# Kernel optimization log

Measured on AMD Instinct MI355X. Metric: run time of the kernel, lower is better.

## Reference

```python
import jax, jax.numpy as jnp
import numpy as np

B, L, D_MODEL = 8, 2048, 768
D_INNER, D_STATE, DT_RANK, K = 1536, 16, 48, 4


def setup_inputs() -> dict:
    key = jax.random.key(0)
    ks = jax.random.split(key, 9)
    s = 0.02
    return {
        "hidden_states": jax.random.normal(ks[0], (B, L, D_MODEL), jnp.float32),
        "W_in": jax.random.normal(ks[1], (D_MODEL, 2 * D_INNER), jnp.float32) * s,
        "conv_w": jax.random.normal(ks[2], (D_INNER, 1, K), jnp.float32) * s,
        "conv_b": jax.random.normal(ks[3], (D_INNER,), jnp.float32) * s,
        "W_x": jax.random.normal(ks[4], (DT_RANK + 2 * D_STATE, D_INNER), jnp.float32) * s,
        "W_dt": jax.random.normal(ks[5], (D_INNER, DT_RANK), jnp.float32) * s,
        "b_dt": jax.random.normal(ks[6], (D_INNER,), jnp.float32) * s,
        "A_log": jax.random.normal(ks[7], (D_INNER, D_STATE), jnp.float32),
        "D_param": jax.random.normal(ks[8], (D_INNER,), jnp.float32),
    }


def _mamba(hidden_states, W_in, conv_w, conv_b, W_x, W_dt, b_dt, A_log, D_param):
    # in_proj then chunk into ssm branch (x) and gating residual (res)
    xz = hidden_states @ W_in                      # (B, L, 2*d_inner)
    x, res = jnp.split(xz, 2, axis=-1)             # each (B, L, d_inner)

    # causal depthwise conv over time, then SiLU
    xc = x.transpose(0, 2, 1)                      # (B, C, L)
    xc = jax.lax.conv_general_dilated(
        xc, conv_w, window_strides=(1,), padding=[(K - 1, 0)],
        feature_group_count=D_INNER, dimension_numbers=("NCH", "OIH", "NCH"))
    x = jax.nn.silu(xc + conv_b[None, :, None]).transpose(0, 2, 1)  # (B, L, d_inner)

    # input-dependent SSM parameters
    x_dbl = x @ W_x.T                              # (B, L, dt_rank + 2*d_state)
    dt = jax.nn.softplus(x_dbl[..., :DT_RANK] @ W_dt.T + b_dt)      # (B, L, d_inner)
    Bm = x_dbl[..., DT_RANK:DT_RANK + D_STATE]     # (B, L, d_state)
    Cm = x_dbl[..., DT_RANK + D_STATE:]            # (B, L, d_state)
    A = -jnp.exp(A_log)                            # (d_inner, d_state)

    def step(h, inp):
        x_t, dt_t, B_t, C_t = inp                  # (B,d_inner),(B,d_inner),(B,d_state),(B,d_state)
        dA = jnp.exp(dt_t[..., None] * A)          # (B, d_inner, d_state)
        dBx = (dt_t * x_t)[..., None] * B_t[:, None, :]
        h = dA * h + dBx
        y = jnp.einsum("bds,bs->bd", h, C_t)
        return h, y

    xs = (x.transpose(1, 0, 2), dt.transpose(1, 0, 2),
          Bm.transpose(1, 0, 2), Cm.transpose(1, 0, 2))
    h0 = jnp.zeros((x.shape[0], D_INNER, D_STATE), x.dtype)
    _, ys = jax.lax.scan(step, h0, xs)             # ys: (L, B, d_inner)
    y = ys.transpose(1, 0, 2) + x * D_param        # skip term
    return y * jax.nn.silu(res)                    # gated output (B, L, d_inner)


def reference(hidden_states, W_in, conv_w, conv_b, W_x, W_dt, b_dt, A_log, D_param):
    return _mamba(hidden_states, W_in, conv_w, conv_b, W_x, W_dt, b_dt, A_log, D_param)
```

## Files before the change

### kernel.cpp

```cpp
#include <hip/hip_runtime.h>
#include <hip/hip_bf16.h>
#include <stdint.h>

#define B_SZ 8
#define L_SZ 2048
#define DM 768
#define DI 1536
#define DS 16
#define DR 48
#define M_SZ (B_SZ * L_SZ)
#define N1 (2 * DI)

#define NC 32
#define TC (L_SZ / NC)
#define CH (B_SZ * DI)
#define KS 6
#define NT (DM / 64)
#define L2E 1.44269504088896f

typedef short short8 __attribute__((ext_vector_type(8)));
typedef float f32x4 __attribute__((ext_vector_type(4)));
typedef float f32x2 __attribute__((ext_vector_type(2)));

__device__ __forceinline__ ushort f2b(float f) {
  __hip_bfloat16 h = __float2bfloat16(f);
  return *reinterpret_cast<ushort*>(&h);
}
__device__ __forceinline__ float b2f(ushort u) {
  __hip_bfloat16 h;
  *reinterpret_cast<ushort*>(&h) = u;
  return __bfloat162float(h);
}
__device__ __forceinline__ ushort f2h(float f) {
  _Float16 h = (_Float16)f;
  return *reinterpret_cast<ushort*>(&h);
}
__device__ __forceinline__ float h2f(ushort u) {
  _Float16 h;
  *reinterpret_cast<ushort*>(&h) = u;
  return (float)h;
}

__device__ __forceinline__ void gl16(const ushort* g, ushort* l) {
  __builtin_amdgcn_global_load_lds(
      (const __attribute__((address_space(1))) void*)g,
      (__attribute__((address_space(3))) void*)l, 16, 0, 0);
}


__global__ __launch_bounds__(256) void prep_all(const float4* __restrict__ hs4,
                                                const float* __restrict__ w_in,
                                                const float* __restrict__ wx_f,
                                                const float* __restrict__ wdt_f,
                                                ushort4* __restrict__ A1,
                                                ushort* __restrict__ wt,
                                                ushort* __restrict__ wx_b,
                                                ushort* __restrict__ wdt_p) {
  const int n4 = M_SZ * DM / 4;
  const int nT = 3072 * 96;
  const int nwx = 80 * DI;
  const int nwdt = DI * 64;
  int idx = blockIdx.x * 256 + threadIdx.x;
  if (idx < n4) {
    float4 v = hs4[idx];
    ushort4 o;
    o.x = f2b(v.x); o.y = f2b(v.y); o.z = f2b(v.z); o.w = f2b(v.w);
    A1[idx] = o;
  } else if (idx < n4 + nT) {
    int j = idx - n4;
    int n = j % 3072;
    int kb = (j / 3072) * 8;
    short8 o;
#pragma unroll
    for (int q = 0; q < 8; ++q) o[q] = (short)f2b(w_in[(size_t)(kb + q) * 3072 + n]);
    *(short8*)(wt + (size_t)n * DM + kb) = o;
  } else if (idx < n4 + nT + nwx) {
    int j = idx - n4 - nT;
    wx_b[j] = f2b(wx_f[j]);
  } else if (idx < n4 + nT + nwx + nwdt) {
    int j = idx - n4 - nT - nwx;
    int col = j >> 6, k = j & 63;
    wdt_p[j] = (k < DR) ? f2b(wdt_f[col * DR + k]) : (ushort)0;
  }
}


__global__ __launch_bounds__(512, 1) void gemm_xz(const ushort* __restrict__ A,
                                                  const ushort* __restrict__ Bt,
                                                  ushort* __restrict__ xout,
                                                  ushort* __restrict__ gateout) {
  __shared__ ushort lds[65536];

  const int t = threadIdx.x;
  const int lane = t & 63;
  const int wid = t >> 6;
  const int wm = wid >> 2, wn = wid & 3;
  const int r = lane & 15, hi = lane >> 4;

  const int g = blockIdx.x;
  const int swz = (g & 7) * (768 / 8) + (g >> 3);
  const int bx = swz & 63;
  const int by = swz >> 6;
  const int bm = bx * 256;
  const int bn = by * 256;

  const bool isA = wid < 4;
  const int w4 = wid & 3;
  const ushort* gsrc[8];
  int ldso[8];
#pragma unroll
  for (int i = 0; i < 8; ++i) {
    int c = w4 * 8 + i;
    int mg = c >> 1, kkc = c & 1;
    gsrc[i] = (isA ? A + (size_t)(bm + mg * 16 + r) * DM
                   : Bt + (size_t)(bn + mg * 16 + r) * DM) + kkc * 32 + hi * 8;
    ldso[i] = (isA ? 0 : 16384) + c * 512;
  }

  f32x4 acc[8][4];
#pragma unroll
  for (int m = 0; m < 8; ++m)
#pragma unroll
    for (int n = 0; n < 4; ++n) acc[m][n] = f32x4{0.f, 0.f, 0.f, 0.f};

#pragma unroll
  for (int i = 0; i < 8; ++i) gl16(gsrc[i], &lds[ldso[i]]);
  asm volatile("s_waitcnt vmcnt(0)" ::: "memory");
  __builtin_amdgcn_s_barrier();

  for (int kt = 0; kt < NT; ++kt) {
    const int cur = kt & 1;
    const ushort* bufA = &lds[cur * 32768];
    const ushort* bufB = bufA + 16384;
    ushort* nxt = &lds[(cur ^ 1) * 32768];
    const int koff = (kt + 1) * 64;
    const bool more = (kt + 1 < NT);

    short8 afr[4][2], bfr[2][2];
#pragma unroll
    for (int q = 0; q < 4; ++q) {
      const int mq = q >> 1, nq = q & 1;
      if (nq == 0) {
#pragma unroll
        for (int m = 0; m < 4; ++m)
#pragma unroll
          for (int kk = 0; kk < 2; ++kk)
            afr[m][kk] = *(const short8*)&bufA[((wm * 8 + mq * 4 + m) * 2 + kk) * 512 + lane * 8];
      }
#pragma unroll
      for (int n = 0; n < 2; ++n)
#pragma unroll
        for (int kk = 0; kk < 2; ++kk)
          bfr[n][kk] = *(const short8*)&bufB[((wn * 4 + nq * 2 + n) * 2 + kk) * 512 + lane * 8];

      if (more) {
        gl16(gsrc[2 * q] + koff, nxt + ldso[2 * q]);
        gl16(gsrc[2 * q + 1] + koff, nxt + ldso[2 * q + 1]);
      }

      asm volatile("s_barrier" ::: "memory");

      __builtin_amdgcn_s_setprio(1);
#pragma unroll
      for (int m = 0; m < 4; ++m)
#pragma unroll
        for (int n = 0; n < 2; ++n) {
          f32x4 a = acc[mq * 4 + m][nq * 2 + n];
          a = __builtin_amdgcn_mfma_f32_16x16x32_bf16(afr[m][0], bfr[n][0], a, 0, 0, 0);
          a = __builtin_amdgcn_mfma_f32_16x16x32_bf16(afr[m][1], bfr[n][1], a, 0, 0, 0);
          acc[mq * 4 + m][nq * 2 + n] = a;
        }
      __builtin_amdgcn_s_setprio(0);

      if (q == 3) asm volatile("s_waitcnt vmcnt(0)" ::: "memory");
      asm volatile("s_barrier" ::: "memory");
    }
  }

  const bool isx = (bn < DI);
  ushort* outp = isx ? xout : gateout;
  const int cbase = bn - (isx ? 0 : DI) + wn * 64;
#pragma unroll
  for (int mf = 0; mf < 8; ++mf)
#pragma unroll
    for (int nf = 0; nf < 4; ++nf) {
      int col = cbase + nf * 16 + r;
#pragma unroll
      for (int j = 0; j < 4; ++j) {
        int row = bm + wm * 128 + mf * 16 + hi * 4 + j;
        float v = acc[mf][nf][j];
        if (!isx) v = v / (1.f + __expf(-v));
        outp[(size_t)row * DI + col] = f2b(v);
      }
    }
}


__global__ __launch_bounds__(256) void conv_silu(const ushort* __restrict__ xp,
                                                 const float* __restrict__ cw,
                                                 const float* __restrict__ cb,
                                                 ushort* __restrict__ xc) {
  int tid = blockIdx.x * 256 + threadIdx.x;
  const int nd = DI / 8;
  int db = tid % nd;
  int row = tid / nd;
  int d0 = db * 8;
  int l = row & (L_SZ - 1);
  const ushort* base = xp + (size_t)row * DI + d0;
  short8 z8 = {0, 0, 0, 0, 0, 0, 0, 0};
  short8 x0 = *(const short8*)base;
  short8 xm1 = (l >= 1) ? *(const short8*)(base - DI) : z8;
  short8 xm2 = (l >= 2) ? *(const short8*)(base - 2 * DI) : z8;
  short8 xm3 = (l >= 3) ? *(const short8*)(base - 3 * DI) : z8;
  short8 o;
#pragma unroll
  for (int j = 0; j < 8; ++j) {
    float4 w = *(const float4*)(cw + (size_t)(d0 + j) * 4);
    float a = cb[d0 + j] + w.x * b2f((ushort)xm3[j]) + w.y * b2f((ushort)xm2[j]) +
              w.z * b2f((ushort)xm1[j]) + w.w * b2f((ushort)x0[j]);
    float s = a / (1.f + __expf(-a));
    o[j] = (short)f2b(s);
  }
  *(short8*)(xc + (size_t)row * DI + d0) = o;
}


__global__ __launch_bounds__(256) void xdbl_gemm(const ushort* __restrict__ xc,
                                                 const ushort* __restrict__ wx,
                                                 float* __restrict__ xdp) {
  int wave = blockIdx.x * 4 + (threadIdx.x >> 6);
  int ks = blockIdx.y;
  int lane = threadIdx.x & 63;
  int r = lane & 15, hi = lane >> 4;
  int row0 = wave * 16;
  f32x4 acc[5];
#pragma unroll
  for (int n = 0; n < 5; ++n) acc[n] = f32x4{0.f, 0.f, 0.f, 0.f};
  const int kbeg = ks * (DI / KS), kend = kbeg + DI / KS;
  for (int k0 = kbeg; k0 < kend; k0 += 32) {
    short8 a = *(const short8*)(xc + (size_t)(row0 + r) * DI + k0 + hi * 8);
#pragma unroll
    for (int n = 0; n < 5; ++n) {
      short8 b = *(const short8*)(wx + (size_t)(n * 16 + r) * DI + k0 + hi * 8);
      acc[n] = __builtin_amdgcn_mfma_f32_16x16x32_bf16(a, b, acc[n], 0, 0, 0);
    }
  }
  float* op = xdp + (size_t)ks * M_SZ * 80;
#pragma unroll
  for (int n = 0; n < 5; ++n)
#pragma unroll
    for (int j = 0; j < 4; ++j)
      op[(size_t)(row0 + hi * 4 + j) * 80 + n * 16 + r] = acc[n][j];
}

__global__ __launch_bounds__(256) void reduce_xd(const float4* __restrict__ xdp,
                                                 float4* __restrict__ xd) {
  int i = blockIdx.x * 256 + threadIdx.x;
  if (i >= M_SZ * 20) return;
  float4 s = xdp[i];
#pragma unroll
  for (int k = 1; k < KS; ++k) {
    float4 v = xdp[(size_t)k * M_SZ * 20 + i];
    s.x += v.x; s.y += v.y; s.z += v.z; s.w += v.w;
  }
  xd[i] = s;
}


__device__ __forceinline__ short8 pack8f(const float* p) {
  short8 v;
#pragma unroll
  for (int i = 0; i < 8; ++i) v[i] = (short)f2b(p[i]);
  return v;
}

__global__ __launch_bounds__(256) void dt_gemm(const float* __restrict__ xd,
                                               const ushort* __restrict__ wdtp,
                                               const float* __restrict__ bdt,
                                               ushort* __restrict__ dt) {
  int wave = blockIdx.x * 4 + (threadIdx.x >> 6);
  int lane = threadIdx.x & 63;
  int r = lane & 15, hi = lane >> 4;
  int row0 = wave * 16;
  int c0 = blockIdx.y * 64;

  float atmp[8];
  const float* ap = xd + (size_t)(row0 + r) * 80 + hi * 8;
  float4 q0 = *(const float4*)ap, q1 = *(const float4*)(ap + 4);
  atmp[0] = q0.x; atmp[1] = q0.y; atmp[2] = q0.z; atmp[3] = q0.w;
  atmp[4] = q1.x; atmp[5] = q1.y; atmp[6] = q1.z; atmp[7] = q1.w;
  short8 a0 = pack8f(atmp);
  short8 a1 = {0, 0, 0, 0, 0, 0, 0, 0};
  if (hi < 2) {
    const float* ap1 = xd + (size_t)(row0 + r) * 80 + 32 + hi * 8;
    float4 p0 = *(const float4*)ap1, p1 = *(const float4*)(ap1 + 4);
    atmp[0] = p0.x; atmp[1] = p0.y; atmp[2] = p0.z; atmp[3] = p0.w;
    atmp[4] = p1.x; atmp[5] = p1.y; atmp[6] = p1.z; atmp[7] = p1.w;
    a1 = pack8f(atmp);
  }

  f32x4 acc[4];
#pragma unroll
  for (int n = 0; n < 4; ++n) acc[n] = f32x4{0.f, 0.f, 0.f, 0.f};
#pragma unroll
  for (int n = 0; n < 4; ++n) {
    const ushort* wp = wdtp + (size_t)(c0 + n * 16 + r) * 64;
    short8 b0 = *(const short8*)(wp + hi * 8);
    short8 b1 = *(const short8*)(wp + 32 + hi * 8);
    acc[n] = __builtin_amdgcn_mfma_f32_16x16x32_bf16(a0, b0, acc[n], 0, 0, 0);
    acc[n] = __builtin_amdgcn_mfma_f32_16x16x32_bf16(a1, b1, acc[n], 0, 0, 0);
  }
#pragma unroll
  for (int n = 0; n < 4; ++n)
#pragma unroll
    for (int j = 0; j < 4; ++j) {
      int col = c0 + n * 16 + r;
      float z = acc[n][j] + bdt[col];
      float sp = (z > 20.f) ? z : __logf(1.f + __expf(z));
      dt[(size_t)(row0 + hi * 4 + j) * DI + col] = f2h(sp);
    }
}


__global__ __launch_bounds__(256) void scan_pass1(const ushort* __restrict__ dt,
                                                  const ushort* __restrict__ xc,
                                                  const float* __restrict__ xd,
                                                  const float* __restrict__ A_log,
                                                  float* __restrict__ hend,
                                                  float* __restrict__ sumdt) {
  const int d = blockIdx.x * 256 + threadIdx.x;
  const int c = blockIdx.y, b = blockIdx.z;
  const int t0 = c * TC;

  __shared__ float Bs[TC * 16];
  for (int i = threadIdx.x; i < TC * 16; i += 256) {
    int tt = i >> 4, s = i & 15;
    Bs[i] = xd[((size_t)(b * L_SZ + t0 + tt)) * 80 + DR + s];
  }

  f32x2 a2[8];
  const float4* al4 = (const float4*)(A_log + (size_t)d * DS);
#pragma unroll
  for (int q = 0; q < 4; ++q) {
    float4 v = al4[q];
    a2[2 * q] = f32x2{-__expf(v.x) * L2E, -__expf(v.y) * L2E};
    a2[2 * q + 1] = f32x2{-__expf(v.z) * L2E, -__expf(v.w) * L2E};
  }

  __syncthreads();

  f32x2 h2[8];
#pragma unroll
  for (int s = 0; s < 8; ++s) h2[s] = f32x2{0.f, 0.f};
  float sd = 0.f;

  const ushort* dtp = dt + ((size_t)b * L_SZ + t0) * DI + d;
  const ushort* xp = xc + ((size_t)b * L_SZ + t0) * DI + d;

  ushort dtu_n = dtp[0];
  ushort xu_n = xp[0];
  for (int tt = 0; tt < TC; ++tt) {
    ushort dtu = dtu_n;
    ushort xu = xu_n;
    dtu_n = dtp[(size_t)(tt + 1) * DI];
    xu_n = xp[(size_t)(tt + 1) * DI];
    float dtv = h2f(dtu);
    float xv = b2f(xu);
    sd += dtv;
    float dx = dtv * xv;
    f32x2 dt2 = f32x2{dtv, dtv};
    f32x2 dx2 = f32x2{dx, dx};
    const f32x2* bp2 = (const f32x2*)&Bs[tt * 16];
#pragma unroll
    for (int sp = 0; sp < 8; ++sp) {
      f32x2 arg = dt2 * a2[sp];
      float e0, e1;
      asm("v_exp_f32 %0, %1" : "=v"(e0) : "v"(arg[0]));
      asm("v_exp_f32 %0, %1" : "=v"(e1) : "v"(arg[1]));
      f32x2 dA = f32x2{e0, e1};
      h2[sp] = dA * h2[sp] + dx2 * bp2[sp];
    }
  }

  const size_t ch = (size_t)b * DI + d;
  sumdt[ch * NC + c] = sd;
  float4* hp = (float4*)&hend[((size_t)c * CH + ch) * 16];
#pragma unroll
  for (int q = 0; q < 4; ++q)
    hp[q] = make_float4(h2[2 * q][0], h2[2 * q][1], h2[2 * q + 1][0], h2[2 * q + 1][1]);
}

__global__ __launch_bounds__(256) void scan_pass2(const float* __restrict__ A_log,
                                                  const float* __restrict__ sumdt,
                                                  const float* __restrict__ hend,
                                                  float* __restrict__ hstart) {
  int idx = blockIdx.x * 256 + threadIdx.x;
  int ch = idx >> 4, s = idx & 15;
  int d = ch % DI;
  float A = -__expf(A_log[d * DS + s]);
  float h = 0.f;
  for (int c = 0; c < NC; ++c) {
    hstart[((size_t)c * CH + ch) * 16 + s] = h;
    float sd = sumdt[(size_t)ch * NC + c];
    h = __expf(A * sd) * h + hend[((size_t)c * CH + ch) * 16 + s];
  }
}

__global__ __launch_bounds__(256) void scan_pass3(const ushort* __restrict__ dt,
                                                  const ushort* __restrict__ xc,
                                                  const float* __restrict__ xd,
                                                  const ushort* __restrict__ gateb,
                                                  const float* __restrict__ A_log,
                                                  const float* __restrict__ Dp,
                                                  const float* __restrict__ hstart,
                                                  float* __restrict__ out) {
  const int d = blockIdx.x * 256 + threadIdx.x;
  const int c = blockIdx.y, b = blockIdx.z;
  const int t0 = c * TC;

  __shared__ float Bs[TC * 16];
  __shared__ float Cs[TC * 16];
  for (int i = threadIdx.x; i < TC * 16; i += 256) {
    int tt = i >> 4, s = i & 15;
    size_t row = ((size_t)(b * L_SZ + t0 + tt)) * 80;
    Bs[i] = xd[row + DR + s];
    Cs[i] = xd[row + DR + DS + s];
  }

  f32x2 a2[8];
  const float4* al4 = (const float4*)(A_log + (size_t)d * DS);
#pragma unroll
  for (int q = 0; q < 4; ++q) {
    float4 v = al4[q];
    a2[2 * q] = f32x2{-__expf(v.x) * L2E, -__expf(v.y) * L2E};
    a2[2 * q + 1] = f32x2{-__expf(v.z) * L2E, -__expf(v.w) * L2E};
  }
  const float Dpv = Dp[d];

  const size_t ch = (size_t)b * DI + d;
  f32x2 h2[8];
  const float4* hp = (const float4*)&hstart[((size_t)c * CH + ch) * 16];
#pragma unroll
  for (int q = 0; q < 4; ++q) {
    float4 v = hp[q];
    h2[2 * q] = f32x2{v.x, v.y};
    h2[2 * q + 1] = f32x2{v.z, v.w};
  }

  __syncthreads();

  const ushort* dtp = dt + ((size_t)b * L_SZ + t0) * DI + d;
  const ushort* xp = xc + ((size_t)b * L_SZ + t0) * DI + d;
  const ushort* gp = gateb + ((size_t)b * L_SZ + t0) * DI + d;
  float* op = out + ((size_t)b * L_SZ + t0) * DI + d;

  ushort dtu_n = dtp[0];
  ushort xu_n = xp[0];
  ushort gu_n = gp[0];
  for (int tt = 0; tt < TC; ++tt) {
    ushort dtu = dtu_n;
    ushort xu = xu_n;
    ushort gu = gu_n;
    dtu_n = dtp[(size_t)(tt + 1) * DI];
    xu_n = xp[(size_t)(tt + 1) * DI];
    gu_n = gp[(size_t)(tt + 1) * DI];
    float dtv = h2f(dtu);
    float xv = b2f(xu);
    float gv = b2f(gu);
    float dx = dtv * xv;
    f32x2 dt2 = f32x2{dtv, dtv};
    f32x2 dx2 = f32x2{dx, dx};
    const f32x2* bp2 = (const f32x2*)&Bs[tt * 16];
    const f32x2* cp2 = (const f32x2*)&Cs[tt * 16];
    f32x2 ya = f32x2{0.f, 0.f}, yb = f32x2{0.f, 0.f};
#pragma unroll
    for (int sp = 0; sp < 8; sp += 2) {
      f32x2 arg0 = dt2 * a2[sp];
      f32x2 arg1 = dt2 * a2[sp + 1];
      float e0, e1, e2, e3;
      asm("v_exp_f32 %0, %1" : "=v"(e0) : "v"(arg0[0]));
      asm("v_exp_f32 %0, %1" : "=v"(e1) : "v"(arg0[1]));
      asm("v_exp_f32 %0, %1" : "=v"(e2) : "v"(arg1[0]));
      asm("v_exp_f32 %0, %1" : "=v"(e3) : "v"(arg1[1]));
      f32x2 dA0 = f32x2{e0, e1};
      f32x2 dA1 = f32x2{e2, e3};
      h2[sp] = dA0 * h2[sp] + dx2 * bp2[sp];
      h2[sp + 1] = dA1 * h2[sp + 1] + dx2 * bp2[sp + 1];
      ya = ya + h2[sp] * cp2[sp];
      yb = yb + h2[sp + 1] * cp2[sp + 1];
    }
    f32x2 ys = ya + yb;
    float y = ys[0] + ys[1];
    op[(size_t)tt * DI] = (y + xv * Dpv) * gv;
  }
}


extern "C" void kernel_launch(void* const* d_in, const int* in_sizes, int n_in,
                              void* d_out, int out_size, void* d_ws, size_t ws_size,
                              hipStream_t stream) {
  const float* hs     = (const float*)d_in[0];
  const float* W_in   = (const float*)d_in[1];
  const float* conv_w = (const float*)d_in[2];
  const float* conv_b = (const float*)d_in[3];
  const float* W_x    = (const float*)d_in[4];
  const float* W_dt   = (const float*)d_in[5];
  const float* b_dt   = (const float*)d_in[6];
  const float* A_log  = (const float*)d_in[7];
  const float* D_par  = (const float*)d_in[8];
  float* out = (float*)d_out;
  char* ws = (char*)d_ws;

  size_t o = 0;
  ushort* A1   = (ushort*)(ws + o); o += (size_t)M_SZ * DM * 2;
  ushort* Wt1  = (ushort*)(ws + o); o += (size_t)N1 * DM * 2;
  ushort* xpre = (ushort*)(ws + o); o += (size_t)M_SZ * DI * 2;
  ushort* gate = (ushort*)(ws + o); o += (size_t)M_SZ * DI * 2;
  ushort* xcv  = (ushort*)(ws + o); o += (size_t)M_SZ * DI * 2;
  float*  xdbl = (float*)(ws + o);  o += (size_t)M_SZ * 80 * 4;
  ushort* dtb  = (ushort*)(ws + o); o += (size_t)M_SZ * DI * 2;
  float*  xdp  = (float*)(ws + o);  o += (size_t)KS * M_SZ * 80 * 4;
  ushort* Wxb  = (ushort*)(ws + o); o += (size_t)80 * DI * 2;
  ushort* Wdtp = (ushort*)(ws + o); o += (size_t)DI * 64 * 2;
  if (ws_size < o) return;

  float* hend   = (float*)(ws + 0);
  float* hstart = (float*)(ws + (size_t)NC * CH * 16 * 4);
  float* sumdt  = (float*)(ws + (size_t)2 * NC * CH * 16 * 4);

  const int nprep = M_SZ * DM / 4 + 3072 * 96 + 80 * DI + DI * 64;
  prep_all<<<dim3((nprep + 255) / 256), dim3(256), 0, stream>>>(
      (const float4*)hs, W_in, W_x, W_dt, (ushort4*)A1, Wt1, Wxb, Wdtp);

  gemm_xz<<<dim3((M_SZ / 256) * (N1 / 256)), dim3(512), 0, stream>>>(A1, Wt1, xpre, gate);

  conv_silu<<<dim3(M_SZ * DI / 8 / 256), dim3(256), 0, stream>>>(xpre, conv_w, conv_b, xcv);

  xdbl_gemm<<<dim3(M_SZ / 64, KS), dim3(256), 0, stream>>>(xcv, Wxb, xdp);
  reduce_xd<<<dim3((M_SZ * 20 + 255) / 256), dim3(256), 0, stream>>>((const float4*)xdp, (float4*)xdbl);

  dt_gemm<<<dim3(M_SZ / 64, 24), dim3(256), 0, stream>>>(xdbl, Wdtp, b_dt, dtb);

  scan_pass1<<<dim3(DI / 256, NC, B_SZ), dim3(256), 0, stream>>>(dtb, xcv, xdbl, A_log, hend, sumdt);
  scan_pass2<<<dim3(CH * 16 / 256), dim3(256), 0, stream>>>(A_log, sumdt, hend, hstart);
  scan_pass3<<<dim3(DI / 256, NC, B_SZ), dim3(256), 0, stream>>>(dtb, xcv, xdbl, gate,
                                                                 A_log, D_par, hstart, out);
}
```

Before: 427.5 us.

## Batch GEMM prefetch issue and rework scan loops with float4 vectors and pointer increments

In the GEMM main loop, all eight global-to-LDS prefetch loads for the next K tile are now issued in the first quarter-iteration instead of two per quarter. The idea is to start memory traffic earlier so it overlaps more of the MFMA work. The scan kernels switch from paired float2 state to float4 vectors and replace indexed addressing with incrementing pointers. Both changes aim to cut address arithmetic and instruction count in the serial recurrence. Front-loading the loads may raise memory-queue pressure and make the later barriers wait longer.

```diff
diff --git a/kernel.cpp b/kernel.cpp
--- a/kernel.cpp
+++ b/kernel.cpp
@@ -20,7 +20,6 @@
 
 typedef short short8 __attribute__((ext_vector_type(8)));
 typedef float f32x4 __attribute__((ext_vector_type(4)));
-typedef float f32x2 __attribute__((ext_vector_type(2)));
 
 __device__ __forceinline__ ushort f2b(float f) {
   __hip_bfloat16 h = __float2bfloat16(f);
@@ -46,6 +45,16 @@
       (const __attribute__((address_space(1))) void*)g,
       (__attribute__((address_space(3))) void*)l, 16, 0, 0);
 }
+
+#define EXP4(dst, src)                                      \
+  {                                                         \
+    float _e0, _e1, _e2, _e3;                               \
+    asm("v_exp_f32 %0, %1" : "=v"(_e0) : "v"((src)[0]));    \
+    asm("v_exp_f32 %0, %1" : "=v"(_e1) : "v"((src)[1]));    \
+    asm("v_exp_f32 %0, %1" : "=v"(_e2) : "v"((src)[2]));    \
+    asm("v_exp_f32 %0, %1" : "=v"(_e3) : "v"((src)[3]));    \
+    (dst) = f32x4{_e0, _e1, _e2, _e3};                      \
+  }
 
 
 __global__ __launch_bounds__(256) void prep_all(const float4* __restrict__ hs4,
@@ -153,9 +162,9 @@
         for (int kk = 0; kk < 2; ++kk)
           bfr[n][kk] = *(const short8*)&bufB[((wn * 4 + nq * 2 + n) * 2 + kk) * 512 + lane * 8];
 
-      if (more) {
-        gl16(gsrc[2 * q] + koff, nxt + ldso[2 * q]);
-        gl16(gsrc[2 * q + 1] + koff, nxt + ldso[2 * q + 1]);
+      if (q == 0 && more) {
+#pragma unroll
+        for (int i = 0; i < 8; ++i) gl16(gsrc[i] + koff, nxt + ldso[i]);
       }
 
       asm volatile("s_barrier" ::: "memory");
@@ -338,56 +347,55 @@
     Bs[i] = xd[((size_t)(b * L_SZ + t0 + tt)) * 80 + DR + s];
   }
 
-  f32x2 a2[8];
+  f32x4 a4[4];
   const float4* al4 = (const float4*)(A_log + (size_t)d * DS);
 #pragma unroll
   for (int q = 0; q < 4; ++q) {
     float4 v = al4[q];
-    a2[2 * q] = f32x2{-__expf(v.x) * L2E, -__expf(v.y) * L2E};
-    a2[2 * q + 1] = f32x2{-__expf(v.z) * L2E, -__expf(v.w) * L2E};
+    a4[q] = f32x4{-__expf(v.x) * L2E, -__expf(v.y) * L2E,
+                  -__expf(v.z) * L2E, -__expf(v.w) * L2E};
   }
 
   __syncthreads();
 
-  f32x2 h2[8];
-#pragma unroll
-  for (int s = 0; s < 8; ++s) h2[s] = f32x2{0.f, 0.f};
+  f32x4 h4[4];
+#pragma unroll
+  for (int q = 0; q < 4; ++q) h4[q] = f32x4{0.f, 0.f, 0.f, 0.f};
   float sd = 0.f;
 
   const ushort* dtp = dt + ((size_t)b * L_SZ + t0) * DI + d;
   const ushort* xp = xc + ((size_t)b * L_SZ + t0) * DI + d;
 
-  ushort dtu_n = dtp[0];
-  ushort xu_n = xp[0];
+  ushort dtu_n = *dtp;
+  ushort xu_n = *xp;
+  const f32x4* bp4 = (const f32x4*)Bs;
   for (int tt = 0; tt < TC; ++tt) {
+    dtp += DI; xp += DI;
     ushort dtu = dtu_n;
     ushort xu = xu_n;
-    dtu_n = dtp[(size_t)(tt + 1) * DI];
-    xu_n = xp[(size_t)(tt + 1) * DI];
+    dtu_n = *dtp;
+    xu_n = *xp;
     float dtv = h2f(dtu);
     float xv = b2f(xu);
     sd += dtv;
     float dx = dtv * xv;
-    f32x2 dt2 = f32x2{dtv, dtv};
-    f32x2 dx2 = f32x2{dx, dx};
-    const f32x2* bp2 = (const f32x2*)&Bs[tt * 16];
-#pragma unroll
-    for (int sp = 0; sp < 8; ++sp) {
-      f32x2 arg = dt2 * a2[sp];
-      float e0, e1;
-      asm("v_exp_f32 %0, %1" : "=v"(e0) : "v"(arg[0]));
-      asm("v_exp_f32 %0, %1" : "=v"(e1) : "v"(arg[1]));
-      f32x2 dA = f32x2{e0, e1};
-      h2[sp] = dA * h2[sp] + dx2 * bp2[sp];
+    f32x4 dts = f32x4{dtv, dtv, dtv, dtv};
+    f32x4 dxs = f32x4{dx, dx, dx, dx};
+#pragma unroll
+    for (int q = 0; q < 4; ++q) {
+      f32x4 arg = dts * a4[q];
+      f32x4 dA;
+      EXP4(dA, arg);
+      h4[q] = dA * h4[q] + dxs * bp4[q];
     }
+    bp4 += 4;
   }
 
   const size_t ch = (size_t)b * DI + d;
   sumdt[ch * NC + c] = sd;
-  float4* hp = (float4*)&hend[((size_t)c * CH + ch) * 16];
-#pragma unroll
-  for (int q = 0; q < 4; ++q)
-    hp[q] = make_float4(h2[2 * q][0], h2[2 * q][1], h2[2 * q + 1][0], h2[2 * q + 1][1]);
+  f32x4* hp = (f32x4*)&hend[((size_t)c * CH + ch) * 16];
+#pragma unroll
+  for (int q = 0; q < 4; ++q) hp[q] = h4[q];
 }
 
 __global__ __launch_bounds__(256) void scan_pass2(const float* __restrict__ A_log,
@@ -427,25 +435,21 @@
     Cs[i] = xd[row + DR + DS + s];
   }
 
-  f32x2 a2[8];
+  f32x4 a4[4];
   const float4* al4 = (const float4*)(A_log + (size_t)d * DS);
 #pragma unroll
   for (int q = 0; q < 4; ++q) {
     float4 v = al4[q];
-    a2[2 * q] = f32x2{-__expf(v.x) * L2E, -__expf(v.y) * L2E};
-    a2[2 * q + 1] = f32x2{-__expf(v.z) * L2E, -__expf(v.w) * L2E};
+    a4[q] = f32x4{-__expf(v.x) * L2E, -__expf(v.y) * L2E,
+                  -__expf(v.z) * L2E, -__expf(v.w) * L2E};
   }
   const float Dpv = Dp[d];
 
   const size_t ch = (size_t)b * DI + d;
-  f32x2 h2[8];
-  const float4* hp = (const float4*)&hstart[((size_t)c * CH + ch) * 16];
-#pragma unroll
-  for (int q = 0; q < 4; ++q) {
-    float4 v = hp[q];
-    h2[2 * q] = f32x2{v.x, v.y};
-    h2[2 * q + 1] = f32x2{v.z, v.w};
-  }
+  f32x4 h4[4];
+  const f32x4* hp = (const f32x4*)&hstart[((size_t)c * CH + ch) * 16];
+#pragma unroll
+  for (int q = 0; q < 4; ++q) h4[q] = hp[q];
 
   __syncthreads();
 
@@ -454,44 +458,38 @@
   const ushort* gp = gateb + ((size_t)b * L_SZ + t0) * DI + d;
   float* op = out + ((size_t)b * L_SZ + t0) * DI + d;
 
-  ushort dtu_n = dtp[0];
-  ushort xu_n = xp[0];
-  ushort gu_n = gp[0];
+  ushort dtu_n = *dtp;
+  ushort xu_n = *xp;
+  ushort gu_n = *gp;
+  const f32x4* bp4 = (const f32x4*)Bs;
+  const f32x4* cp4 = (const f32x4*)Cs;
   for (int tt = 0; tt < TC; ++tt) {
+    dtp += DI; xp += DI; gp += DI;
     ushort dtu = dtu_n;
     ushort xu = xu_n;
     ushort gu = gu_n;
-    dtu_n = dtp[(size_t)(tt + 1) * DI];
-    xu_n = xp[(size_t)(tt + 1) * DI];
-    gu_n = gp[(size_t)(tt + 1) * DI];
+    dtu_n = *dtp;
+    xu_n = *xp;
+    gu_n = *gp;
     float dtv = h2f(dtu);
     float xv = b2f(xu);
     float gv = b2f(gu);
     float dx = dtv * xv;
-    f32x2 dt2 = f32x2{dtv, dtv};
-    f32x2 dx2 = f32x2{dx, dx};
-    const f32x2* bp2 = (const f32x2*)&Bs[tt * 16];
-    const f32x2* cp2 = (const f32x2*)&Cs[tt * 16];
-    f32x2 ya = f32x2{0.f, 0.f}, yb = f32x2{0.f, 0.f};
-#pragma unroll
-    for (int sp = 0; sp < 8; sp += 2) {
-      f32x2 arg0 = dt2 * a2[sp];
-      f32x2 arg1 = dt2 * a2[sp + 1];
-      float e0, e1, e2, e3;
-      asm("v_exp_f32 %0, %1" : "=v"(e0) : "v"(arg0[0]));
-      asm("v_exp_f32 %0, %1" : "=v"(e1) : "v"(arg0[1]));
-      asm("v_exp_f32 %0, %1" : "=v"(e2) : "v"(arg1[0]));
-      asm("v_exp_f32 %0, %1" : "=v"(e3) : "v"(arg1[1]));
-      f32x2 dA0 = f32x2{e0, e1};
-      f32x2 dA1 = f32x2{e2, e3};
-      h2[sp] = dA0 * h2[sp] + dx2 * bp2[sp];
-      h2[sp + 1] = dA1 * h2[sp + 1] + dx2 * bp2[sp + 1];
-      ya = ya + h2[sp] * cp2[sp];
-      yb = yb + h2[sp + 1] * cp2[sp + 1];
+    f32x4 dts = f32x4{dtv, dtv, dtv, dtv};
+    f32x4 dxs = f32x4{dx, dx, dx, dx};
+    f32x4 y4 = f32x4{0.f, 0.f, 0.f, 0.f};
+#pragma unroll
+    for (int q = 0; q < 4; ++q) {
+      f32x4 arg = dts * a4[q];
+      f32x4 dA;
+      EXP4(dA, arg);
+      h4[q] = dA * h4[q] + dxs * bp4[q];
+      y4 = y4 + h4[q] * cp4[q];
     }
-    f32x2 ys = ya + yb;
-    float y = ys[0] + ys[1];
-    op[(size_t)tt * DI] = (y + xv * Dpv) * gv;
+    bp4 += 4; cp4 += 4;
+    float y = (y4[0] + y4[1]) + (y4[2] + y4[3]);
+    op[0] = (y + xv * Dpv) * gv;
+    op += DI;
   }
 }
 
```

Result: slower. 438.2 us (+2.5%).
